# Kernel optimization log

Measured on AMD Instinct MI355X. Metric: run time of the kernel, lower is better.

## Reference

```python
import jax, jax.numpy as jnp
import numpy as np

D_MODEL = 512
D_STATE = 16
EPS = 1e-8
LN_EPS = 1e-5


def setup_inputs() -> dict:
    key = jax.random.key(0)
    ks = jax.random.split(key, 9)
    B, N = 4, 2048
    x = jax.random.normal(ks[0], (B, N, D_MODEL), dtype=jnp.float32)
    A_log = jax.random.normal(ks[1], (D_STATE,), dtype=jnp.float32) * 0.1 - 1.0
    # xavier_uniform with gain=0.5 for B and C linear weights
    lim_B = 0.5 * np.sqrt(6.0 / (D_MODEL + D_STATE))
    W_B = jax.random.uniform(ks[2], (D_STATE, D_MODEL), jnp.float32, -lim_B, lim_B)
    W_C = jax.random.uniform(ks[3], (D_MODEL, D_STATE), jnp.float32, -lim_B, lim_B)
    D = jax.random.normal(ks[4], (D_MODEL,), dtype=jnp.float32) * 0.01
    lim_g = np.sqrt(1.0 / D_MODEL)  # torch Linear default init
    W_gate = jax.random.uniform(ks[5], (D_MODEL, D_MODEL), jnp.float32, -lim_g, lim_g)
    b_gate = jax.random.uniform(ks[6], (D_MODEL,), jnp.float32, -lim_g, lim_g)
    ln_gamma = jnp.ones((D_MODEL,), jnp.float32)
    ln_beta = jnp.zeros((D_MODEL,), jnp.float32)
    return {"x": x, "A_log": A_log, "W_B": W_B, "W_C": W_C, "D": D,
            "W_gate": W_gate, "b_gate": b_gate, "ln_gamma": ln_gamma, "ln_beta": ln_beta}


def reference(x, A_log, W_B, W_C, D, W_gate, b_gate, ln_gamma, ln_beta):
    Bb, N, Dm = x.shape
    A = -jnp.clip(jnp.exp(A_log), EPS, 10.0)                      # (d_state,)
    dt = 1.0 / N
    A_bar = jnp.exp(dt * A)                                       # (d_state,)
    B_bar = jnp.where(jnp.abs(A) > EPS, (A_bar - 1.0) / (A + EPS),
                      jnp.full_like(A, dt))
    Bu = jnp.einsum('bnm,sm->bns', x, W_B) * B_bar                # (B,N,d_state)
    idx = jnp.arange(N)
    diff = jnp.clip(idx[None, :] - idx[:, None], 0, None)[..., None]  # (N,N,1)
    decay = A_bar[None, None, :] ** diff                          # (N,N,d_state)
    mask = (idx[None, :] >= idx[:, None])[..., None]
    decay = decay * mask.astype(decay.dtype)
    h = jnp.einsum('nms,bns->bms', decay, Bu)                     # (B,N,d_state)
    h = jnp.clip(h, -10.0, 10.0)
    y = jnp.einsum('bns,ms->bnm', h, W_C) + D * x                 # (B,N,d_model)
    gate = jax.nn.sigmoid(jnp.einsum('bnm,km->bnk', x, W_gate) + b_gate)
    y = gate * y + (1.0 - gate) * x
    # LayerNorm (dropout is identity in eval mode)
    mu = jnp.mean(y, axis=-1, keepdims=True)
    var = jnp.var(y, axis=-1, keepdims=True)
    return (y - mu) / jnp.sqrt(var + LN_EPS) * ln_gamma + ln_beta
```

## Files before the change

kernel.cpp:

```cpp
#include <hip/hip_runtime.h>
#include <math.h>
#include <stdint.h>

#define D_MODEL 512
#define D_STATE 16
#define NSEQ    2048
#define NBATCH  4
#define EPSF    1e-8f
#define LN_EPSF 1e-5f
#define DT      (1.0f / 2048.0f)

typedef __attribute__((ext_vector_type(8))) short short8;
typedef __attribute__((ext_vector_type(4))) float floatx4;

__device__ __forceinline__ ushort f2bf(float f) {
    uint32_t u = __float_as_uint(f);
    return (ushort)((u + 0x7fffu + ((u >> 16) & 1u)) >> 16);
}

__global__ __launch_bounds__(256) void kP(const float* __restrict__ x,
                                          const float* __restrict__ A_log,
                                          const float* __restrict__ W_B,
                                          const float* __restrict__ Wg,
                                          ushort* __restrict__ wgb,
                                          float* __restrict__ hL,
                                          float* __restrict__ states) {
    __shared__ float wb[D_STATE][D_MODEL + 4];
    __shared__ float bbars[16], abars[16];
    __shared__ float w4[4][16];
    const int tid = threadIdx.x, lane = tid & 63, wave = tid >> 6;

    if (tid < 64) {
        int i = blockIdx.x * 64 + tid;
        const float4* sp = (const float4*)Wg + (size_t)i * 2;
        float4 a = sp[0], b = sp[1];
        float v[8] = {a.x, a.y, a.z, a.w, b.x, b.y, b.z, b.w};
        short8 o;
        #pragma unroll
        for (int j = 0; j < 8; ++j) o[j] = (short)f2bf(v[j]);
        *(short8*)(wgb + (size_t)i * 8) = o;
    }
    if (tid < 16) {
        float A    = -fminf(fmaxf(expf(A_log[tid]), EPSF), 10.0f);
        float Abar = expf(A * DT);
        abars[tid] = Abar;
        bbars[tid] = (fabsf(A) > EPSF) ? (Abar - 1.0f) / (A + EPSF) : DT;
    }
    __syncthreads();
    for (int i = tid; i < D_STATE * D_MODEL; i += 256) {
        int s = i >> 9, m = i & 511;
        wb[s][m] = W_B[i] * bbars[s];
    }
    __syncthreads();

    const int s    = lane & 15;
    const int q    = lane >> 4;
    const int rloc = q + (wave << 2);
    const int row  = blockIdx.x * 16 + rloc;
    const float* xr = x + (size_t)row * D_MODEL;

    float acc = 0.f;
    #pragma unroll 4
    for (int m = 0; m < D_MODEL; m += 4) {
        float4 xv = *(const float4*)(xr + m);
        float4 wv = *(const float4*)(&wb[s][m]);
        acc += xv.x * wv.x + xv.y * wv.y + xv.z * wv.z + xv.w * wv.w;
    }

    float abar = abars[s];
    float a = abar, b = acc;
    {
        float ap = __shfl_up(a, 16), bp = __shfl_up(b, 16);
        if (lane >= 16) { b = a * bp + b; a = a * ap; }
    }
    {
        float ap = __shfl_up(a, 32), bp = __shfl_up(b, 32);
        if (lane >= 32) { b = a * bp + b; a = a * ap; }
    }
    if (q == 3) w4[wave][s] = b;
    __syncthreads();
    float a4 = abar * abar; a4 = a4 * a4;
    float pb = 0.f;
    for (int w = 0; w < wave; ++w) pb = a4 * pb + w4[w][s];
    float hloc = a * pb + b;

    hL[(size_t)row * D_STATE + s] = hloc;
    if (rloc == 15) states[(size_t)blockIdx.x * D_STATE + s] = hloc;
}

#define CBM 32
#define BKC 64
__global__ __launch_bounds__(512) void kc_fused(
    const float*  __restrict__ x,
    const ushort* __restrict__ Wg,
    const float*  __restrict__ hL,
    const float*  __restrict__ states,
    const float*  __restrict__ A_log,
    const float*  __restrict__ W_C,
    const float*  __restrict__ Dvec,
    const float*  __restrict__ bg,
    const float*  __restrict__ gamma,
    const float*  __restrict__ beta,
    float* __restrict__ out) {
    __shared__ ushort Bsub[512 * BKC];
    __shared__ float  hsf[CBM][D_STATE];
    __shared__ float  red[8][CBM][2];

    const int tid  = threadIdx.x;
    const int lane = tid & 63, wave = tid >> 6;
    const int r0   = blockIdx.x * CBM;
    const int fr   = lane & 15, kg = lane >> 4;
    const int rbase = r0 + (wave >> 2) * 16;
    const int colw  = (wave & 3) * 128;

    short8 afp[8][2];
    #pragma unroll
    for (int t = 0; t < 8; ++t) {
        const float* ap = x + (size_t)(rbase + fr) * D_MODEL + t * 64 + kg * 8;
        float4 u0 = *(const float4*)ap;
        float4 u1 = *(const float4*)(ap + 4);
        float4 v0 = *(const float4*)(ap + 32);
        float4 v1 = *(const float4*)(ap + 36);
        float uu[8] = {u0.x,u0.y,u0.z,u0.w,u1.x,u1.y,u1.z,u1.w};
        float vv[8] = {v0.x,v0.y,v0.z,v0.w,v1.x,v1.y,v1.z,v1.w};
        #pragma unroll
        for (int e = 0; e < 8; ++e) {
            afp[t][0][e] = (short)f2bf(uu[e]);
            afp[t][1][e] = (short)f2bf(vv[e]);
        }
    }

    float* stg = (float*)Bsub;
    const int c0    = (blockIdx.x & 63) * 2;
    const int cbase = (blockIdx.x >> 6) * 128;
    for (int i = tid; i < (c0 + 1) * 16; i += 512)
        stg[i] = states[(size_t)cbase * 16 + i];
    __syncthreads();
    {
        int s = tid & 15, nloc = tid >> 4;
        float A   = -fminf(fmaxf(expf(A_log[s]), EPSF), 10.0f);
        float a16 = expf(A * DT * 16.0f);
        int nch = c0 + (nloc >> 4);
        float p = 0.f;
        for (int cc = 0; cc < nch; ++cc) p = a16 * p + stg[cc * 16 + s];
        float hv = expf(A * DT * (float)((nloc & 15) + 1)) * p
                 + hL[(size_t)(r0 + nloc) * D_STATE + s];
        hsf[nloc][s] = fminf(fmaxf(hv, -10.f), 10.f);
    }

    floatx4 acc[8] = {};
    #pragma unroll
    for (int t = 0; t < 8; ++t) {
        __syncthreads();
        #pragma unroll
        for (int is = 0; is < 8; ++is) {
            int row_ = is * 64 + (tid >> 3);
            int g_   = (tid & 7) ^ (row_ & 7);
            const ushort* gsrc_ = Wg + (size_t)row_ * D_MODEL + t * 64 + g_ * 8;
            __builtin_amdgcn_global_load_lds(
                (const __attribute__((address_space(1))) void*)gsrc_,
                (__attribute__((address_space(3))) void*)((char*)Bsub + is * 8192 + tid * 16),
                16, 0, 0);
        }
        __syncthreads();

        #pragma unroll
        for (int j = 0; j < 8; ++j) {
            int rb = colw + j * 16 + fr;
            short8 b0 = *(const short8*)(Bsub + (size_t)rb * BKC + (((kg    ) ^ (rb & 7)) * 8));
            short8 b1 = *(const short8*)(Bsub + (size_t)rb * BKC + (((kg + 4) ^ (rb & 7)) * 8));
            acc[j] = __builtin_amdgcn_mfma_f32_16x16x32_bf16(afp[t][0], b0, acc[j], 0, 0, 0);
            acc[j] = __builtin_amdgcn_mfma_f32_16x16x32_bf16(afp[t][1], b1, acc[j], 0, 0, 0);
        }
    }

    float vsum[4] = {}, vsq[4] = {};
    #pragma unroll
    for (int j = 0; j < 8; ++j) {
        int col = colw + j * 16 + fr;
        float dv = Dvec[col], bgv = bg[col];
        const float4* wcp = (const float4*)(W_C + (size_t)col * D_STATE);
        float4 w0 = wcp[0], w1 = wcp[1], w2 = wcp[2], w3 = wcp[3];
        #pragma unroll
        for (int q = 0; q < 4; ++q) {
            int rloc = (wave >> 2) * 16 + kg * 4 + q;
            float xv = x[(size_t)(r0 + rloc) * D_MODEL + col];
            const float* hp = hsf[rloc];
            float yv = dv * xv
                + hp[0]*w0.x + hp[1]*w0.y + hp[2]*w0.z + hp[3]*w0.w
                + hp[4]*w1.x + hp[5]*w1.y + hp[6]*w1.z + hp[7]*w1.w
                + hp[8]*w2.x + hp[9]*w2.y + hp[10]*w2.z + hp[11]*w2.w
                + hp[12]*w3.x + hp[13]*w3.y + hp[14]*w3.z + hp[15]*w3.w;
            float lg = acc[j][q] + bgv;
            float gt = 1.f / (1.f + expf(-lg));
            float v  = gt * yv + (1.f - gt) * xv;
            acc[j][q] = v;
            vsum[q] += v;
            vsq[q]  += v * v;
        }
    }
    #pragma unroll
    for (int off = 1; off < 16; off <<= 1) {
        #pragma unroll
        for (int q = 0; q < 4; ++q) {
            vsum[q] += __shfl_xor(vsum[q], off);
            vsq[q]  += __shfl_xor(vsq[q], off);
        }
    }
    if (fr == 0) {
        #pragma unroll
        for (int q = 0; q < 4; ++q) {
            int rloc = (wave >> 2) * 16 + kg * 4 + q;
            red[wave][rloc][0] = vsum[q];
            red[wave][rloc][1] = vsq[q];
        }
    }
    __syncthreads();
    float mu[4], rs[4];
    #pragma unroll
    for (int q = 0; q < 4; ++q) {
        int rloc = (wave >> 2) * 16 + kg * 4 + q;
        int wg0  = (wave >> 2) * 4;
        float s = 0.f, ss = 0.f;
        #pragma unroll
        for (int w = 0; w < 4; ++w) {
            s  += red[wg0 + w][rloc][0];
            ss += red[wg0 + w][rloc][1];
        }
        float m   = s * (1.f / (float)D_MODEL);
        float var = ss * (1.f / (float)D_MODEL) - m * m;
        mu[q] = m;
        rs[q] = rsqrtf(var + LN_EPSF);
    }
    #pragma unroll
    for (int j = 0; j < 8; ++j) {
        int col = colw + j * 16 + fr;
        float ga = gamma[col], be = beta[col];
        #pragma unroll
        for (int q = 0; q < 4; ++q) {
            int rloc = (wave >> 2) * 16 + kg * 4 + q;
            out[(size_t)(r0 + rloc) * D_MODEL + col] =
                (acc[j][q] - mu[q]) * rs[q] * ga + be;
        }
    }
}

extern "C" void kernel_launch(void* const* d_in, const int* in_sizes, int n_in,
                              void* d_out, int out_size, void* d_ws, size_t ws_size,
                              hipStream_t stream) {
    const float* x     = (const float*)d_in[0];
    const float* A_log = (const float*)d_in[1];
    const float* W_B   = (const float*)d_in[2];
    const float* W_C   = (const float*)d_in[3];
    const float* Dv    = (const float*)d_in[4];
    const float* Wg    = (const float*)d_in[5];
    const float* bg    = (const float*)d_in[6];
    const float* gamma = (const float*)d_in[7];
    const float* beta  = (const float*)d_in[8];
    float* out = (float*)d_out;

    const int rows = NBATCH * NSEQ;

    ushort* wgb    = (ushort*)d_ws;
    float*  hL     = (float*)(wgb + (size_t)D_MODEL * D_MODEL);
    float*  states = hL + (size_t)rows * D_STATE;

    hipLaunchKernelGGL(kP, dim3(rows / 16), dim3(256), 0, stream,
                       x, A_log, W_B, Wg, wgb, hL, states);
    hipLaunchKernelGGL(kc_fused, dim3(rows / CBM), dim3(512), 0, stream,
                       x, wgb, hL, states, A_log, W_C, Dv, bg, gamma, beta, out);
}
```

Before: 50.40 us.

## Split gate GEMM by column quarters with resident weight slice; move LayerNorm to separate kernel

The fused kernel is retiled so each block handles 128 rows by 128 output columns and loads its whole 128x512 bf16 slice of the gate weight into LDS once. This replaces the old scheme, which restreamed the full weight per 32-row block with a barrier each k-step. Because a block no longer sees a full row, LayerNorm is split out: the main kernel writes pre-norm values plus per-quarter sum and sum-of-squares partials. A new kernel then reduces those partials and normalizes in place. The cost is an extra launch, a full extra read and write of the output, and 128 KB of LDS per block at 256 blocks.

After: 58.23 us. +15.5%, slower.

```diff
diff --git a/kernel.cpp b/kernel.cpp
--- a/kernel.cpp
+++ b/kernel.cpp
@@ -88,9 +88,7 @@
     if (rloc == 15) states[(size_t)blockIdx.x * D_STATE + s] = hloc;
 }
 
-#define CBM 32
-#define BKC 64
-__global__ __launch_bounds__(512) void kc_fused(
+__global__ __launch_bounds__(512) void kG(
     const float*  __restrict__ x,
     const ushort* __restrict__ Wg,
     const float*  __restrict__ hL,
@@ -99,19 +97,18 @@
     const float*  __restrict__ W_C,
     const float*  __restrict__ Dvec,
     const float*  __restrict__ bg,
-    const float*  __restrict__ gamma,
-    const float*  __restrict__ beta,
+    float* __restrict__ partials,
     float* __restrict__ out) {
-    __shared__ ushort Bsub[512 * BKC];
-    __shared__ float  hsf[CBM][D_STATE];
-    __shared__ float  red[8][CBM][2];
+    __shared__ ushort Wgs[128 * D_MODEL];
+    __shared__ float  hsf[128][D_STATE];
 
     const int tid  = threadIdx.x;
     const int lane = tid & 63, wave = tid >> 6;
-    const int r0   = blockIdx.x * CBM;
+    const int rt   = blockIdx.x >> 2;
+    const int cq   = blockIdx.x & 3;
+    const int r0   = rt * 128;
     const int fr   = lane & 15, kg = lane >> 4;
-    const int rbase = r0 + (wave >> 2) * 16;
-    const int colw  = (wave & 3) * 128;
+    const int rbase = r0 + wave * 16;
 
     short8 afp[8][2];
     #pragma unroll
@@ -130,45 +127,55 @@
         }
     }
 
-    float* stg = (float*)Bsub;
-    const int c0    = (blockIdx.x & 63) * 2;
-    const int cbase = (blockIdx.x >> 6) * 128;
-    for (int i = tid; i < (c0 + 1) * 16; i += 512)
+    float* stg = (float*)Wgs;
+    const int c0    = (rt & 15) * 8;
+    const int cbase = (rt >> 4) * 128;
+    for (int i = tid; i < (c0 + 8) * 16; i += 512)
         stg[i] = states[(size_t)cbase * 16 + i];
     __syncthreads();
     {
-        int s = tid & 15, nloc = tid >> 4;
+        int s = tid & 15;
         float A   = -fminf(fmaxf(expf(A_log[s]), EPSF), 10.0f);
         float a16 = expf(A * DT * 16.0f);
-        int nch = c0 + (nloc >> 4);
-        float p = 0.f;
-        for (int cc = 0; cc < nch; ++cc) p = a16 * p + stg[cc * 16 + s];
-        float hv = expf(A * DT * (float)((nloc & 15) + 1)) * p
-                 + hL[(size_t)(r0 + nloc) * D_STATE + s];
-        hsf[nloc][s] = fminf(fmaxf(hv, -10.f), 10.f);
-    }
+        #pragma unroll
+        for (int it = 0; it < 4; ++it) {
+            int nloc = (tid >> 4) + it * 32;
+            int nch  = c0 + (nloc >> 4);
+            float p = 0.f;
+            for (int cc = 0; cc < nch; ++cc) p = a16 * p + stg[cc * 16 + s];
+            float hv = expf(A * DT * (float)((nloc & 15) + 1)) * p
+                     + hL[(size_t)(r0 + nloc) * D_STATE + s];
+            hsf[nloc][s] = fminf(fmaxf(hv, -10.f), 10.f);
+        }
+    }
+    __syncthreads();
+
+    {
+        const int rloc = tid >> 6;
+        const int si   = tid & 63;
+        const int t_   = si >> 3, sg = si & 7;
+        #pragma unroll
+        for (int is = 0; is < 16; ++is) {
+            int r  = is * 8 + rloc;
+            int g  = sg ^ (r & 7);
+            const ushort* gsrc = Wg + (size_t)(cq * 128 + r) * D_MODEL + t_ * 64 + g * 8;
+            __builtin_amdgcn_global_load_lds(
+                (const __attribute__((address_space(1))) void*)gsrc,
+                (__attribute__((address_space(3))) void*)((char*)Wgs + is * 8192 + tid * 16),
+                16, 0, 0);
+        }
+    }
+    __syncthreads();
 
     floatx4 acc[8] = {};
     #pragma unroll
     for (int t = 0; t < 8; ++t) {
-        __syncthreads();
-        #pragma unroll
-        for (int is = 0; is < 8; ++is) {
-            int row_ = is * 64 + (tid >> 3);
-            int g_   = (tid & 7) ^ (row_ & 7);
-            const ushort* gsrc_ = Wg + (size_t)row_ * D_MODEL + t * 64 + g_ * 8;
-            __builtin_amdgcn_global_load_lds(
-                (const __attribute__((address_space(1))) void*)gsrc_,
-                (__attribute__((address_space(3))) void*)((char*)Bsub + is * 8192 + tid * 16),
-                16, 0, 0);
-        }
-        __syncthreads();
-
         #pragma unroll
         for (int j = 0; j < 8; ++j) {
-            int rb = colw + j * 16 + fr;
-            short8 b0 = *(const short8*)(Bsub + (size_t)rb * BKC + (((kg    ) ^ (rb & 7)) * 8));
-            short8 b1 = *(const short8*)(Bsub + (size_t)rb * BKC + (((kg + 4) ^ (rb & 7)) * 8));
+            int rb = j * 16 + fr;
+            const ushort* base = Wgs + (size_t)rb * D_MODEL;
+            short8 b0 = *(const short8*)(base + (t * 8 + ((kg    ) ^ (rb & 7))) * 8);
+            short8 b1 = *(const short8*)(base + (t * 8 + ((kg + 4) ^ (rb & 7))) * 8);
             acc[j] = __builtin_amdgcn_mfma_f32_16x16x32_bf16(afp[t][0], b0, acc[j], 0, 0, 0);
             acc[j] = __builtin_amdgcn_mfma_f32_16x16x32_bf16(afp[t][1], b1, acc[j], 0, 0, 0);
         }
@@ -177,13 +184,13 @@
     float vsum[4] = {}, vsq[4] = {};
     #pragma unroll
     for (int j = 0; j < 8; ++j) {
-        int col = colw + j * 16 + fr;
+        int col = cq * 128 + j * 16 + fr;
         float dv = Dvec[col], bgv = bg[col];
         const float4* wcp = (const float4*)(W_C + (size_t)col * D_STATE);
         float4 w0 = wcp[0], w1 = wcp[1], w2 = wcp[2], w3 = wcp[3];
         #pragma unroll
         for (int q = 0; q < 4; ++q) {
-            int rloc = (wave >> 2) * 16 + kg * 4 + q;
+            int rloc = wave * 16 + kg * 4 + q;
             float xv = x[(size_t)(r0 + rloc) * D_MODEL + col];
             const float* hp = hsf[rloc];
             float yv = dv * xv
@@ -200,6 +207,13 @@
         }
     }
     #pragma unroll
+    for (int j = 0; j < 8; ++j) {
+        int col = cq * 128 + j * 16 + fr;
+        #pragma unroll
+        for (int q = 0; q < 4; ++q)
+            out[(size_t)(r0 + wave * 16 + kg * 4 + q) * D_MODEL + col] = acc[j][q];
+    }
+    #pragma unroll
     for (int off = 1; off < 16; off <<= 1) {
         #pragma unroll
         for (int q = 0; q < 4; ++q) {
@@ -210,39 +224,49 @@
     if (fr == 0) {
         #pragma unroll
         for (int q = 0; q < 4; ++q) {
-            int rloc = (wave >> 2) * 16 + kg * 4 + q;
-            red[wave][rloc][0] = vsum[q];
-            red[wave][rloc][1] = vsq[q];
-        }
-    }
-    __syncthreads();
-    float mu[4], rs[4];
-    #pragma unroll
-    for (int q = 0; q < 4; ++q) {
-        int rloc = (wave >> 2) * 16 + kg * 4 + q;
-        int wg0  = (wave >> 2) * 4;
-        float s = 0.f, ss = 0.f;
-        #pragma unroll
-        for (int w = 0; w < 4; ++w) {
-            s  += red[wg0 + w][rloc][0];
-            ss += red[wg0 + w][rloc][1];
-        }
-        float m   = s * (1.f / (float)D_MODEL);
-        float var = ss * (1.f / (float)D_MODEL) - m * m;
-        mu[q] = m;
-        rs[q] = rsqrtf(var + LN_EPSF);
-    }
-    #pragma unroll
-    for (int j = 0; j < 8; ++j) {
-        int col = colw + j * 16 + fr;
-        float ga = gamma[col], be = beta[col];
-        #pragma unroll
-        for (int q = 0; q < 4; ++q) {
-            int rloc = (wave >> 2) * 16 + kg * 4 + q;
-            out[(size_t)(r0 + rloc) * D_MODEL + col] =
-                (acc[j][q] - mu[q]) * rs[q] * ga + be;
-        }
-    }
+            size_t row = (size_t)(r0 + wave * 16 + kg * 4 + q);
+            partials[((size_t)cq * 8192 + row) * 2 + 0] = vsum[q];
+            partials[((size_t)cq * 8192 + row) * 2 + 1] = vsq[q];
+        }
+    }
+}
+
+__global__ __launch_bounds__(256) void kLN(const float* __restrict__ partials,
+                                           const float* __restrict__ gamma,
+                                           const float* __restrict__ beta,
+                                           float* __restrict__ out) {
+    const int tid  = threadIdx.x;
+    const int lane = tid & 63, wave = tid >> 6;
+    const size_t row = (size_t)blockIdx.x * 4 + wave;
+
+    float s = 0.f, ss = 0.f;
+    #pragma unroll
+    for (int cqq = 0; cqq < 4; ++cqq) {
+        s  += partials[((size_t)cqq * 8192 + row) * 2 + 0];
+        ss += partials[((size_t)cqq * 8192 + row) * 2 + 1];
+    }
+    const float mu = s * (1.f / (float)D_MODEL);
+    const float var = ss * (1.f / (float)D_MODEL) - mu * mu;
+    const float rs = rsqrtf(var + LN_EPSF);
+
+    const int col0 = lane * 8;
+    float* op = out + row * D_MODEL + col0;
+    float4 v0 = *(float4*)op;
+    float4 v1 = *(float4*)(op + 4);
+    float4 g0 = *(const float4*)(gamma + col0);
+    float4 g1 = *(const float4*)(gamma + col0 + 4);
+    float4 b0 = *(const float4*)(beta + col0);
+    float4 b1 = *(const float4*)(beta + col0 + 4);
+    v0.x = (v0.x - mu) * rs * g0.x + b0.x;
+    v0.y = (v0.y - mu) * rs * g0.y + b0.y;
+    v0.z = (v0.z - mu) * rs * g0.z + b0.z;
+    v0.w = (v0.w - mu) * rs * g0.w + b0.w;
+    v1.x = (v1.x - mu) * rs * g1.x + b1.x;
+    v1.y = (v1.y - mu) * rs * g1.y + b1.y;
+    v1.z = (v1.z - mu) * rs * g1.z + b1.z;
+    v1.w = (v1.w - mu) * rs * g1.w + b1.w;
+    *(float4*)op = v0;
+    *(float4*)(op + 4) = v1;
 }
 
 extern "C" void kernel_launch(void* const* d_in, const int* in_sizes, int n_in,
@@ -261,12 +285,15 @@
 
     const int rows = NBATCH * NSEQ;
 
-    ushort* wgb    = (ushort*)d_ws;
-    float*  hL     = (float*)(wgb + (size_t)D_MODEL * D_MODEL);
-    float*  states = hL + (size_t)rows * D_STATE;
+    ushort* wgb      = (ushort*)d_ws;
+    float*  hL       = (float*)(wgb + (size_t)D_MODEL * D_MODEL);
+    float*  states   = hL + (size_t)rows * D_STATE;
+    float*  partials = states + (size_t)512 * D_STATE;
 
     hipLaunchKernelGGL(kP, dim3(rows / 16), dim3(256), 0, stream,
                        x, A_log, W_B, Wg, wgb, hL, states);
-    hipLaunchKernelGGL(kc_fused, dim3(rows / CBM), dim3(512), 0, stream,
-                       x, wgb, hL, states, A_log, W_C, Dv, bg, gamma, beta, out);
-}
+    hipLaunchKernelGGL(kG, dim3(256), dim3(512), 0, stream,
+                       x, wgb, hL, states, A_log, W_C, Dv, bg, partials, out);
+    hipLaunchKernelGGL(kLN, dim3(rows / 4), dim3(256), 0, stream,
+                       partials, gamma, beta, out);
+}
```
